# Kernel tuning notes

Measured on AMD Instinct MI355X. Metric: run time of the kernel, lower is better.

## Reference

```python
import jax, jax.numpy as jnp
import numpy as np

# Module hyperparameters
P_, K_, NH = 8, 4, 8
B, H, W, C = 2, 64, 24, 256


def setup_inputs() -> dict:
    key = jax.random.key(0)
    ks = jax.random.split(key, 16)

    def w(k, shape, s=0.02):
        return (jax.random.normal(k, shape) * s).astype(jnp.float32)

    z = lambda *shape: jnp.zeros(shape, jnp.float32)
    return {
        'x_2d': jax.random.normal(ks[0], (B, H, W, C), dtype=jnp.float32),
        # block projections (used as x @ W + b)
        'wq_proj': w(ks[1], (C, C)), 'bq_proj': z(C),
        'wk_proj': w(ks[2], (C, C)), 'bk_proj': z(C),
        'wv_proj': w(ks[3], (C, C)), 'bv_proj': z(C),
        # routing attention projections
        'wq_a': w(ks[4], (C, C)), 'bq_a': z(C),
        'wk_a': w(ks[5], (C, C)), 'bk_a': z(C),
        'wv_a': w(ks[6], (C, C)), 'bv_a': z(C),
        'wo_a': w(ks[7], (C, C)), 'bo_a': z(C),
        # global conv path (HWIO, 5x5, SAME padding == torch padding=2)
        'conv_w': w(ks[8], (5, 5, C, C)), 'conv_b': z(C),
        # layer norms
        'ln1_g': jnp.ones((C,), jnp.float32), 'ln1_b': z(C),
        'ln2_g': jnp.ones((C,), jnp.float32), 'ln2_b': z(C),
    }


def _layer_norm(t, g, b, eps=1e-5):
    m = t.mean(-1, keepdims=True)
    v = ((t - m) ** 2).mean(-1, keepdims=True)
    return (t - m) / jnp.sqrt(v + eps) * g + b


def reference(x_2d, wq_proj, bq_proj, wk_proj, bk_proj, wv_proj, bv_proj,
              wq_a, bq_a, wk_a, bk_a, wv_a, bv_a, wo_a, bo_a,
              conv_w, conv_b, ln1_g, ln1_b, ln2_g, ln2_b):
    Bb, Hh, Ww, Cc = x_2d.shape
    hp = Hh // P_                      # block height
    dk = Cc // NH
    kv = min(K_, P_)

    x_p = x_2d.reshape(Bb, P_, hp, Ww, Cc)
    q_p = x_p @ wq_proj + bq_proj
    k_p = x_p @ wk_proj + bk_proj
    v_p = x_p @ wv_proj + bv_proj

    # block-level routing: mean-pooled block descriptors -> top-k blocks
    q_loc = q_p.mean((2, 3))           # [B,P,C]
    k_loc = k_p.mean((2, 3))
    S_loc = jnp.einsum('bpc,bqc->bpq', q_loc, k_loc)
    _, R = jax.lax.top_k(S_loc, kv)    # [B,P,kv] int32 indices into P

    # gather routed K/V blocks: [B,P,kv,hp*W,C]
    k_flat = k_p.reshape(Bb, P_, hp * Ww, Cc)
    v_flat = v_p.reshape(Bb, P_, hp * Ww, Cc)
    k_fil = jax.vmap(lambda t, r: t[r])(k_flat, R).reshape(Bb, P_, kv, hp, Ww, Cc)
    v_fil = jax.vmap(lambda t, r: t[r])(v_flat, R).reshape(Bb, P_, kv, hp, Ww, Cc)
    q_un = jnp.broadcast_to(q_p[:, :, None], (Bb, P_, kv, hp, Ww, Cc))

    # multi-head attention over flattened (kv*hp*W) per block p
    L = kv * hp * Ww
    def to_heads(t, w, b):
        t = t @ w + b
        t = t.reshape(Bb, P_, kv, hp, Ww, NH, dk)
        return t.transpose(0, 5, 1, 2, 3, 4, 6).reshape(Bb, NH, P_, L, dk)

    qh = to_heads(q_un, wq_a, bq_a)
    kh = to_heads(k_fil, wk_a, bk_a)
    vh = to_heads(v_fil, wv_a, bv_a)

    scores = jnp.einsum('bhpqd,bhpkd->bhpqk', qh, kh) / jnp.sqrt(jnp.float32(dk))
    attn = jax.nn.softmax(scores, axis=-1)
    ctx = jnp.einsum('bhpqk,bhpkd->bhpqd', attn, vh)
    # 'b h p (k hp w) dk -> b p k hp w (h dk)'
    ctx = ctx.reshape(Bb, NH, P_, kv, hp, Ww, dk).transpose(0, 2, 3, 4, 5, 1, 6)
    ctx = ctx.reshape(Bb, P_, kv, hp, Ww, Cc)
    routing_out = (ctx @ wo_a + bo_a).mean(2)          # [B,P,hp,W,C]

    x_res = _layer_norm(x_p + routing_out, ln1_g, ln1_b)

    # global conv path (NHWC SAME conv, kernel 5)
    kv_g = (k_p + v_p).reshape(Bb, Hh, Ww, Cc)
    g = jax.lax.conv_general_dilated(kv_g, conv_w, (1, 1), 'SAME',
                                     dimension_numbers=('NHWC', 'HWIO', 'NHWC')) + conv_b
    g = g.reshape(Bb, P_, hp, Ww, Cc)

    out = _layer_norm(x_res + g, ln2_g, ln2_b)
    return out.reshape(Bb, Hh, Ww, Cc)
```

## Files before the change

### kernel.cpp

```cpp
#include <hip/hip_runtime.h>
#include <hip/hip_bf16.h>


#define NPOS 3072
#define CD   256
#define NE   (NPOS*CD)

typedef short bf16x8 __attribute__((ext_vector_type(8)));
typedef float f32x4  __attribute__((ext_vector_type(4)));

__device__ inline ushort f2bf(float f) {
    __hip_bfloat16 h = __float2bfloat16(f);
    return *reinterpret_cast<ushort*>(&h);
}
__device__ inline float bf2f(ushort u) {
    unsigned v = ((unsigned)u) << 16;
    return *reinterpret_cast<float*>(&v);
}
__device__ inline bf16x8 addbf(bf16x8 a, bf16x8 b) {
    bf16x8 o;
    #pragma unroll
    for (int j = 0; j < 8; ++j)
        o[j] = (short)f2bf(bf2f((ushort)a[j]) + bf2f((ushort)b[j]));
    return o;
}

__global__ __launch_bounds__(256) void wtrans_qkloc(
    const float* __restrict__ w0, const float* __restrict__ w1, const float* __restrict__ w2,
    const float* __restrict__ w3, const float* __restrict__ w4, const float* __restrict__ w5,
    const float* __restrict__ w6, const float* __restrict__ cw,
    ushort* __restrict__ wt, ushort* __restrict__ wct,
    const float* __restrict__ x,
    const float* __restrict__ wq, const float* __restrict__ bq,
    const float* __restrict__ wk, const float* __restrict__ bk,
    float* __restrict__ qloc, float* __restrict__ kloc)
{
    __shared__ float l[64*65];
    int blk = blockIdx.x;
    int tid = threadIdx.x;
    if (blk < 512) {
        const float* M;
        ushort* D;
        int r2;
        if (blk < 112) {
            int mat = blk >> 4; r2 = blk & 15;
            M = mat==0?w0:mat==1?w1:mat==2?w2:mat==3?w3:mat==4?w4:mat==5?w5:w6;
            D = wt + (size_t)mat*65536;
        } else {
            int b2 = blk - 112;
            int tap = b2 >> 4; r2 = b2 & 15;
            M = cw + (size_t)tap*65536;
            D = wct + (size_t)tap*65536;
        }
        int ci0 = (r2 >> 2)*64, co0 = (r2 & 3)*64;
        int a = tid >> 6, c = tid & 63;
        #pragma unroll 4
        for (int k = 0; k < 16; ++k) {
            int cil = k*4 + a;
            l[cil*65 + c] = M[(size_t)(ci0 + cil)*256 + co0 + c];
        }
        __syncthreads();
        #pragma unroll 4
        for (int k = 0; k < 16; ++k) {
            int col = k*4 + a;
            D[((size_t)(co0 + col))*256 + ci0 + c] = f2bf(l[c*65 + col]);
        }
    } else {
        int q2 = blk - 512;
        int bp = q2 & 15, which = q2 >> 4;
        int c = tid;
        float s = 0.f;
        for (int i = 0; i < 192; ++i)
            s += x[((size_t)(bp*192 + i))*256 + c];
        l[c] = s * (1.0f/192.0f);
        __syncthreads();
        const float* W  = which ? wk : wq;
        const float* Bv = which ? bk : bq;
        float* dst      = which ? kloc : qloc;
        float acc = Bv[c];
        #pragma unroll 8
        for (int k = 0; k < 256; ++k)
            acc += l[k] * W[(size_t)k*256 + c];
        dst[bp*256 + c] = acc;
    }
}

__global__ void topk_kern(const float* __restrict__ qloc, const float* __restrict__ kloc,
                          int* __restrict__ Rix)
{
    __shared__ float S[64];
    int b = blockIdx.x, t = threadIdx.x;
    int p = t >> 3, qq = t & 7;
    float s = 0.f;
    for (int c = 0; c < 256; ++c)
        s += qloc[(b*8+p)*256 + c] * kloc[(b*8+qq)*256 + c];
    S[t] = s;
    __syncthreads();
    if (t < 8) {
        float vals[8];
        #pragma unroll
        for (int j = 0; j < 8; ++j) vals[j] = S[t*8 + j];
        for (int j = 0; j < 4; ++j) {
            int best = 0; float bv = vals[0];
            #pragma unroll
            for (int i = 1; i < 8; ++i) if (vals[i] > bv) { bv = vals[i]; best = i; }
            Rix[(b*8 + t)*4 + j] = best;
            vals[best] = -1e30f;
        }
    }
}

__global__ __launch_bounds__(256) void gemm_btx3(
    const float* __restrict__ A,
    const ushort* __restrict__ T0, const ushort* __restrict__ T1, const ushort* __restrict__ T2,
    const float* __restrict__ B0, const float* __restrict__ B1, const float* __restrict__ B2,
    ushort* __restrict__ U0, ushort* __restrict__ U1, ushort* __restrict__ U2)
{
    __shared__ __align__(16) ushort As[32*264];
    int y = blockIdx.y;
    const ushort* T = y==0 ? T0 : (y==1 ? T1 : T2);
    const float* Bi = y==0 ? B0 : (y==1 ? B1 : B2);
    ushort* U = y==0 ? U0 : (y==1 ? U1 : U2);
    int tid = threadIdx.x;
    int m0 = (blockIdx.x >> 1)*32;
    int nh = blockIdx.x & 1;
    #pragma unroll
    for (int i = 0; i < 4; ++i) {
        int c = i*256 + tid;
        int pos = c >> 5, off = (c & 31)*8;
        const float* src = A + (size_t)(m0 + pos)*256 + off;
        float4 v0 = *(const float4*)src;
        float4 v1 = *(const float4*)(src + 4);
        ushort4 o0, o1;
        o0.x = f2bf(v0.x); o0.y = f2bf(v0.y); o0.z = f2bf(v0.z); o0.w = f2bf(v0.w);
        o1.x = f2bf(v1.x); o1.y = f2bf(v1.y); o1.z = f2bf(v1.z); o1.w = f2bf(v1.w);
        *(ushort4*)&As[pos*264 + off]     = o0;
        *(ushort4*)&As[pos*264 + off + 4] = o1;
    }
    __syncthreads();
    int w = tid >> 6, lane = tid & 63, lm = lane & 15, lq = lane >> 4;
    const ushort* tb = T + ((size_t)(nh*128 + w*32 + lm))*256 + lq*8;

    f32x4 acc[2][2];
    #pragma unroll
    for (int mt = 0; mt < 2; ++mt)
        #pragma unroll
        for (int nt = 0; nt < 2; ++nt) acc[mt][nt] = (f32x4){0.f,0.f,0.f,0.f};

    bf16x8 bw[2];
    #pragma unroll
    for (int nt = 0; nt < 2; ++nt) bw[nt] = *(const bf16x8*)(tb + nt*4096);

    for (int kc = 0; kc < 8; ++kc) {
        int nk = (kc + 1 < 8) ? kc + 1 : 7;
        bf16x8 bn[2];
        #pragma unroll
        for (int nt = 0; nt < 2; ++nt) bn[nt] = *(const bf16x8*)(tb + nt*4096 + nk*32);
        bf16x8 af[2];
        #pragma unroll
        for (int mt = 0; mt < 2; ++mt)
            af[mt] = *(const bf16x8*)&As[(mt*16 + lm)*264 + kc*32 + lq*8];
        #pragma unroll
        for (int mt = 0; mt < 2; ++mt)
            #pragma unroll
            for (int nt = 0; nt < 2; ++nt)
                acc[mt][nt] = __builtin_amdgcn_mfma_f32_16x16x32_bf16(af[mt], bw[nt], acc[mt][nt], 0,0,0);
        #pragma unroll
        for (int nt = 0; nt < 2; ++nt) bw[nt] = bn[nt];
    }

    #pragma unroll
    for (int mt = 0; mt < 2; ++mt) {
        #pragma unroll
        for (int nt = 0; nt < 2; ++nt) {
            int n = nh*128 + w*32 + nt*16 + lm;
            float bb = Bi[n];
            #pragma unroll
            for (int j = 0; j < 4; ++j) {
                int m = m0 + mt*16 + lq*4 + j;
                U[(size_t)m*256 + n] = f2bf(acc[mt][nt][j] + bb);
            }
        }
    }
}

__global__ __launch_bounds__(256) void gemm_bt3(
    const ushort* __restrict__ A0, const ushort* __restrict__ A1, const ushort* __restrict__ A2,
    const ushort* __restrict__ T0, const ushort* __restrict__ T1, const ushort* __restrict__ T2,
    const float* __restrict__ B0, const float* __restrict__ B1, const float* __restrict__ B2,
    ushort* __restrict__ U0, ushort* __restrict__ U1, ushort* __restrict__ U2,
    float s0, float s1, float s2)
{
    __shared__ __align__(16) ushort As[32*264];
    int y = blockIdx.y;
    const ushort* A = y==0 ? A0 : (y==1 ? A1 : A2);
    const ushort* T = y==0 ? T0 : (y==1 ? T1 : T2);
    const float* Bi = y==0 ? B0 : (y==1 ? B1 : B2);
    ushort* U = y==0 ? U0 : (y==1 ? U1 : U2);
    float  sc = y==0 ? s0 : (y==1 ? s1 : s2);
    int tid = threadIdx.x;
    int m0 = (blockIdx.x >> 1)*32;
    int nh = blockIdx.x & 1;
    #pragma unroll
    for (int i = 0; i < 4; ++i) {
        int c = i*256 + tid;
        int pos = c >> 5, off = (c & 31)*8;
        *(bf16x8*)&As[pos*264 + off] = *(const bf16x8*)(A + (size_t)(m0 + pos)*256 + off);
    }
    __syncthreads();
    int w = tid >> 6, lane = tid & 63, lm = lane & 15, lq = lane >> 4;
    const ushort* tb = T + ((size_t)(nh*128 + w*32 + lm))*256 + lq*8;

    f32x4 acc[2][2];
    #pragma unroll
    for (int mt = 0; mt < 2; ++mt)
        #pragma unroll
        for (int nt = 0; nt < 2; ++nt) acc[mt][nt] = (f32x4){0.f,0.f,0.f,0.f};

    bf16x8 bw[2];
    #pragma unroll
    for (int nt = 0; nt < 2; ++nt) bw[nt] = *(const bf16x8*)(tb + nt*4096);

    for (int kc = 0; kc < 8; ++kc) {
        int nk = (kc + 1 < 8) ? kc + 1 : 7;
        bf16x8 bn[2];
        #pragma unroll
        for (int nt = 0; nt < 2; ++nt) bn[nt] = *(const bf16x8*)(tb + nt*4096 + nk*32);
        bf16x8 af[2];
        #pragma unroll
        for (int mt = 0; mt < 2; ++mt)
            af[mt] = *(const bf16x8*)&As[(mt*16 + lm)*264 + kc*32 + lq*8];
        #pragma unroll
        for (int mt = 0; mt < 2; ++mt)
            #pragma unroll
            for (int nt = 0; nt < 2; ++nt)
                acc[mt][nt] = __builtin_amdgcn_mfma_f32_16x16x32_bf16(af[mt], bw[nt], acc[mt][nt], 0,0,0);
        #pragma unroll
        for (int nt = 0; nt < 2; ++nt) bw[nt] = bn[nt];
    }

    #pragma unroll
    for (int mt = 0; mt < 2; ++mt) {
        #pragma unroll
        for (int nt = 0; nt < 2; ++nt) {
            int n = nh*128 + w*32 + nt*16 + lm;
            float bb = Bi[n];
            #pragma unroll
            for (int j = 0; j < 4; ++j) {
                int m = m0 + mt*16 + lq*4 + j;
                U[(size_t)m*256 + n] = f2bf((acc[mt][nt][j] + bb) * sc);
            }
        }
    }
}

__global__ __launch_bounds__(256) void attn_conv(
    const ushort* __restrict__ qab, const ushort* __restrict__ kab,
    const ushort* __restrict__ vab, const int* __restrict__ Rix,
    float* __restrict__ pl, ushort* __restrict__ pacc,
    const ushort* __restrict__ kpb, const ushort* __restrict__ vpb,
    const ushort* __restrict__ wct, ushort* __restrict__ pconv)
{
    __shared__ __align__(16) ushort SMEM[19008];
    int tid = threadIdx.x;
    int bid = blockIdx.x;
    if (bid < 640) {
        int ch = bid & 1;
        int t2 = bid >> 1;
        int rp = t2 / 5, dy = t2 - rp*5;
        int b = rp >> 5, y0 = (rp & 31)*2;

        const bf16x8 zero8 = (bf16x8){0,0,0,0,0,0,0,0};
        #pragma unroll
        for (int i = 0; i < 7; ++i) {
            int c = i*256 + tid;
            int row = (c >= 896);
            int cc = c - row*896;
            int pos = cc >> 5, off = (cc & 31)*8;
            int y = y0 + row + dy - 2;
            bf16x8 v = zero8;
            if (y >= 0 && y < 64 && pos >= 2 && pos < 26) {
                size_t sb = ((size_t)((b*64 + y)*24 + (pos - 2)))*256 + off;
                v = addbf(*(const bf16x8*)(kpb + sb), *(const bf16x8*)(vpb + sb));
            }
            *(bf16x8*)(&SMEM[row*9504 + pos*264 + off]) = v;
        }
        __syncthreads();

        int w = tid >> 6;
        int lane = tid & 63, lm = lane & 15, lq = lane >> 4;
        const ushort* bbase = wct + ((size_t)((dy*5)*256 + ch*128 + w*32 + lm))*256 + lq*8;
        const ushort* a00 = &SMEM[lm*264 + lq*8];

        f32x4 acc[2][2][2];
        #pragma unroll
        for (int r = 0; r < 2; ++r)
            #pragma unroll
            for (int mt = 0; mt < 2; ++mt)
                #pragma unroll
                for (int nt = 0; nt < 2; ++nt)
                    acc[r][mt][nt] = (f32x4){0.f,0.f,0.f,0.f};

        bf16x8 b0[2], b1[2];
        #pragma unroll
        for (int nt = 0; nt < 2; ++nt) b0[nt] = *(const bf16x8*)(bbase + nt*4096);
        #pragma unroll
        for (int nt = 0; nt < 2; ++nt) b1[nt] = *(const bf16x8*)(bbase + 32 + nt*4096);

        for (int iter = 0; iter < 40; ++iter) {
            int i2 = (iter + 2 < 40) ? iter + 2 : 39;
            int boff = (i2 >> 3)*65536 + (i2 & 7)*32;
            bf16x8 bn[2];
            #pragma unroll
            for (int nt = 0; nt < 2; ++nt) bn[nt] = *(const bf16x8*)(bbase + boff + nt*4096);

            int aoff = (iter >> 3)*264 + (iter & 7)*32;
            bf16x8 af[2][2];
            #pragma unroll
            for (int r = 0; r < 2; ++r)
                #pragma unroll
                for (int mt = 0; mt < 2; ++mt)
                    af[r][mt] = *(const bf16x8*)(a00 + r*9504 + mt*4224 + aoff);

            #pragma unroll
            for (int r = 0; r < 2; ++r)
                #pragma unroll
                for (int mt = 0; mt < 2; ++mt)
                    #pragma unroll
                    for (int nt = 0; nt < 2; ++nt)
                        acc[r][mt][nt] = __builtin_amdgcn_mfma_f32_16x16x32_bf16(
                            af[r][mt], b0[nt], acc[r][mt][nt], 0, 0, 0);

            #pragma unroll
            for (int nt = 0; nt < 2; ++nt) { b0[nt] = b1[nt]; b1[nt] = bn[nt]; }
        }

        #pragma unroll
        for (int r = 0; r < 2; ++r) {
            int grow = rp*2 + r;
            #pragma unroll
            for (int mt = 0; mt < 2; ++mt) {
                #pragma unroll
                for (int nt = 0; nt < 2; ++nt) {
                    int cob = ch*128 + w*32 + nt*16 + lm;
                    #pragma unroll
                    for (int j = 0; j < 4; ++j) {
                        int x = mt*16 + lq*4 + j;
                        if (x < 24)
                            pconv[((size_t)(dy*3072 + grow*24 + x))*256 + cob]
                                = f2bf(acc[r][mt][nt][j]);
                    }
                }
            }
        }
    } else {
        int id = bid - 640;
        int bph = id >> 2, kvb = id & 3;
        int w = tid >> 6, lane = tid & 63;
        int lm = lane & 15, lq = lane >> 4;
        int bp = bph >> 3, h = bph & 7, b = bp >> 3;
        int r = Rix[bp*4 + kvb];
        int vrow0 = (b*8 + r)*192;
        ushort* P  = SMEM;
        ushort* Vs = SMEM + 2560;

        #pragma unroll
        for (int i = 0; i < 6; ++i) {
            int idx = i*256 + tid;
            int pos = idx >> 3, c4 = (idx & 7)*4;
            ushort4 v = *(const ushort4*)(vab + ((size_t)(vrow0 + pos))*256 + h*32 + c4);
            Vs[(c4+0)*200 + pos] = v.x;
            Vs[(c4+1)*200 + pos] = v.y;
            Vs[(c4+2)*200 + pos] = v.z;
            Vs[(c4+3)*200 + pos] = v.w;
        }

        bf16x8 qf[3];
        #pragma unroll
        for (int t = 0; t < 3; ++t)
            qf[t] = *(const bf16x8*)(qab + ((size_t)(bp*192 + w*48 + t*16 + lm))*256 + h*32 + lq*8);

        const ushort* kbase = kab + ((size_t)(vrow0))*256 + h*32 + lq*8;
        ushort* pw = P + w*640;
        __syncthreads();

        f32x4 O[3][2];
        #pragma unroll
        for (int t = 0; t < 3; ++t) { O[t][0] = (f32x4){0,0,0,0}; O[t][1] = (f32x4){0,0,0,0}; }
        float l[3] = {0.f, 0.f, 0.f};

        for (int k0 = 0; k0 < 192; k0 += 32) {
            bf16x8 kf0 = *(const bf16x8*)(kbase + (size_t)(k0 + lm)*256);
            bf16x8 kf1 = *(const bf16x8*)(kbase + (size_t)(k0 + 16 + lm)*256);
            bf16x8 vf0 = *(const bf16x8*)(&Vs[lm*200 + k0 + lq*8]);
            bf16x8 vf1 = *(const bf16x8*)(&Vs[(16 + lm)*200 + k0 + lq*8]);
            #pragma unroll
            for (int t = 0; t < 3; ++t) {
                f32x4 s0 = __builtin_amdgcn_mfma_f32_16x16x32_bf16(kf0, qf[t], (f32x4){0,0,0,0}, 0,0,0);
                f32x4 s1 = __builtin_amdgcn_mfma_f32_16x16x32_bf16(kf1, qf[t], (f32x4){0,0,0,0}, 0,0,0);
                float p0[4], p1[4];
                #pragma unroll
                for (int j = 0; j < 4; ++j) { p0[j] = __expf(s0[j]); p1[j] = __expf(s1[j]); }
                l[t] += p0[0]+p0[1]+p0[2]+p0[3] + p1[0]+p1[1]+p1[2]+p1[3];
                ushort4 a, c;
                a.x = f2bf(p0[0]); a.y = f2bf(p0[1]); a.z = f2bf(p0[2]); a.w = f2bf(p0[3]);
                c.x = f2bf(p1[0]); c.y = f2bf(p1[1]); c.z = f2bf(p1[2]); c.w = f2bf(p1[3]);
                *(ushort4*)(pw + lm*40 + lq*4)      = a;
                *(ushort4*)(pw + lm*40 + 16 + lq*4) = c;
                bf16x8 pf = *(const bf16x8*)(pw + lm*40 + lq*8);
                O[t][0] = __builtin_amdgcn_mfma_f32_16x16x32_bf16(pf, vf0, O[t][0], 0,0,0);
                O[t][1] = __builtin_amdgcn_mfma_f32_16x16x32_bf16(pf, vf1, O[t][1], 0,0,0);
            }
        }

        #pragma unroll
        for (int t = 0; t < 3; ++t) {
            float lt = l[t];
            lt += __shfl_xor(lt, 16);
            lt += __shfl_xor(lt, 32);
            size_t pbase = ((size_t)(bph*4 + kvb))*192 + w*48 + t*16;
            if (lq == 0) pl[pbase + lm] = lt;
            #pragma unroll
            for (int nt = 0; nt < 2; ++nt)
                #pragma unroll
                for (int reg = 0; reg < 4; ++reg)
                    pacc[(pbase + lq*4 + reg)*32 + nt*16 + lm] = f2bf(O[t][nt][reg]);
        }
    }
}

__global__ __launch_bounds__(256) void gemm_wo_ln2(
    const float* __restrict__ pl, const ushort* __restrict__ pacc,
    const ushort* __restrict__ T, const float* __restrict__ boa,
    const float* __restrict__ x,
    const float* __restrict__ g1, const float* __restrict__ b1,
    const ushort* __restrict__ pc, const float* __restrict__ cb,
    const float* __restrict__ g2, const float* __restrict__ b2,
    float* __restrict__ out)
{
    __shared__ __align__(16) ushort As[32*264];
    __shared__ float L2x[32*256];
    int tid = threadIdx.x;
    int m0 = blockIdx.x*32;
    #pragma unroll
    for (int i = 0; i < 4; ++i) {
        int c = i*256 + tid;
        int pos = c >> 5, off = (c & 31)*8;
        int m = m0 + pos;
        int bp = m / 192, q = m - bp*192;
        int h = off >> 5, d0 = off & 31;
        int bph = bp*8 + h;
        float ls = 0.f;
        float cv[8] = {0,0,0,0,0,0,0,0};
        #pragma unroll
        for (int k = 0; k < 4; ++k) {
            size_t pidx = ((size_t)(bph*4 + k))*192 + q;
            ls += pl[pidx];
            bf16x8 pv = *(const bf16x8*)(pacc + pidx*32 + d0);
            #pragma unroll
            for (int j = 0; j < 8; ++j) cv[j] += bf2f((ushort)pv[j]);
        }
        ushort o[8];
        #pragma unroll
        for (int j = 0; j < 8; ++j) o[j] = f2bf(cv[j] / ls);
        *(ushort4*)&As[pos*264 + off]     = make_ushort4(o[0],o[1],o[2],o[3]);
        *(ushort4*)&As[pos*264 + off + 4] = make_ushort4(o[4],o[5],o[6],o[7]);
    }
    __syncthreads();
    int w = tid >> 6, lane = tid & 63, lm = lane & 15, lq = lane >> 4;
    const ushort* tb = T + ((size_t)(w*64 + lm))*256 + lq*8;

    f32x4 acc[2][4];
    #pragma unroll
    for (int mt = 0; mt < 2; ++mt)
        #pragma unroll
        for (int nt = 0; nt < 4; ++nt) acc[mt][nt] = (f32x4){0.f,0.f,0.f,0.f};

    bf16x8 bw[4];
    #pragma unroll
    for (int nt = 0; nt < 4; ++nt) bw[nt] = *(const bf16x8*)(tb + nt*4096);

    for (int kc = 0; kc < 8; ++kc) {
        int nk = (kc + 1 < 8) ? kc + 1 : 7;
        bf16x8 bn[4];
        #pragma unroll
        for (int nt = 0; nt < 4; ++nt) bn[nt] = *(const bf16x8*)(tb + nt*4096 + nk*32);
        bf16x8 af[2];
        #pragma unroll
        for (int mt = 0; mt < 2; ++mt)
            af[mt] = *(const bf16x8*)&As[(mt*16 + lm)*264 + kc*32 + lq*8];
        #pragma unroll
        for (int mt = 0; mt < 2; ++mt)
            #pragma unroll
            for (int nt = 0; nt < 4; ++nt)
                acc[mt][nt] = __builtin_amdgcn_mfma_f32_16x16x32_bf16(af[mt], bw[nt], acc[mt][nt], 0,0,0);
        #pragma unroll
        for (int nt = 0; nt < 4; ++nt) bw[nt] = bn[nt];
    }

    #pragma unroll
    for (int mt = 0; mt < 2; ++mt) {
        #pragma unroll
        for (int nt = 0; nt < 4; ++nt) {
            int n = w*64 + nt*16 + lm;
            float bb = boa[n];
            #pragma unroll
            for (int j = 0; j < 4; ++j) {
                int pos = mt*16 + lq*4 + j;
                float val = acc[mt][nt][j] + bb;
                L2x[pos*256 + n] = val + x[(size_t)(m0 + pos)*256 + n];
            }
        }
    }
    __syncthreads();
    #pragma unroll
    for (int rr = 0; rr < 8; ++rr) {
        int pos = w*8 + rr;
        int grow = m0 + pos;
        float4 a = *(const float4*)(&L2x[pos*256 + lane*4]);
        float x0 = a.x, x1 = a.y, x2 = a.z, x3 = a.w;
        float s  = x0 + x1 + x2 + x3;
        float sq = x0*x0 + x1*x1 + x2*x2 + x3*x3;
        #pragma unroll
        for (int off = 32; off > 0; off >>= 1) {
            s  += __shfl_xor(s,  off);
            sq += __shfl_xor(sq, off);
        }
        float mean = s * (1.0f/256.0f);
        float var  = sq * (1.0f/256.0f) - mean*mean;
        float rstd = rsqrtf(var + 1e-5f);
        float4 gv = *(const float4*)(g1 + lane*4);
        float4 bv = *(const float4*)(b1 + lane*4);
        float r0 = (x0 - mean)*rstd*gv.x + bv.x;
        float r1 = (x1 - mean)*rstd*gv.y + bv.y;
        float r2 = (x2 - mean)*rstd*gv.z + bv.z;
        float r3 = (x3 - mean)*rstd*gv.w + bv.w;
        size_t base = (size_t)grow*256 + lane*4;
        float4 gsum = *(const float4*)(cb + lane*4);
        #pragma unroll
        for (int d = 0; d < 5; ++d) {
            ushort4 v = *(const ushort4*)(pc + (size_t)d*NE + base);
            gsum.x += bf2f(v.x); gsum.y += bf2f(v.y);
            gsum.z += bf2f(v.z); gsum.w += bf2f(v.w);
        }
        float y0 = r0 + gsum.x, y1 = r1 + gsum.y, y2 = r2 + gsum.z, y3 = r3 + gsum.w;
        float s2v  = y0 + y1 + y2 + y3;
        float sq2  = y0*y0 + y1*y1 + y2*y2 + y3*y3;
        #pragma unroll
        for (int off = 32; off > 0; off >>= 1) {
            s2v += __shfl_xor(s2v, off);
            sq2 += __shfl_xor(sq2, off);
        }
        float mean2 = s2v * (1.0f/256.0f);
        float var2  = sq2 * (1.0f/256.0f) - mean2*mean2;
        float rstd2 = rsqrtf(var2 + 1e-5f);
        float4 g2v = *(const float4*)(g2 + lane*4);
        float4 b2v = *(const float4*)(b2 + lane*4);
        float4 o;
        o.x = (y0 - mean2)*rstd2*g2v.x + b2v.x;
        o.y = (y1 - mean2)*rstd2*g2v.y + b2v.y;
        o.z = (y2 - mean2)*rstd2*g2v.z + b2v.z;
        o.w = (y3 - mean2)*rstd2*g2v.w + b2v.w;
        *(float4*)(out + base) = o;
    }
}

extern "C" void kernel_launch(void* const* d_in, const int* in_sizes, int n_in,
                              void* d_out, int out_size, void* d_ws, size_t ws_size,
                              hipStream_t stream)
{
    (void)in_sizes; (void)n_in; (void)out_size; (void)ws_size;
    const float* x    = (const float*)d_in[0];
    const float* wq   = (const float*)d_in[1];
    const float* bq   = (const float*)d_in[2];
    const float* wk   = (const float*)d_in[3];
    const float* bk   = (const float*)d_in[4];
    const float* wv   = (const float*)d_in[5];
    const float* bv   = (const float*)d_in[6];
    const float* wqa  = (const float*)d_in[7];
    const float* bqa  = (const float*)d_in[8];
    const float* wka  = (const float*)d_in[9];
    const float* bka  = (const float*)d_in[10];
    const float* wva  = (const float*)d_in[11];
    const float* bva  = (const float*)d_in[12];
    const float* woa  = (const float*)d_in[13];
    const float* boa  = (const float*)d_in[14];
    const float* cw   = (const float*)d_in[15];
    const float* cbi  = (const float*)d_in[16];
    const float* ln1g = (const float*)d_in[17];
    const float* ln1b = (const float*)d_in[18];
    const float* ln2g = (const float*)d_in[19];
    const float* ln2b = (const float*)d_in[20];
    float* out = (float*)d_out;

    float* ws = (float*)d_ws;
    const size_t HNE = NE/2;
    ushort* qpb = (ushort*)(ws + 0*HNE);
    ushort* kpb = (ushort*)(ws + 1*HNE);
    ushort* vpb = (ushort*)(ws + 3*HNE);
    ushort* qab = (ushort*)(ws + 4*HNE);
    ushort* kab = (ushort*)(ws + 5*HNE);
    ushort* vab = (ushort*)(ws + 6*HNE);
    float* R    = ws + 8*HNE;
    ushort* pacc = (ushort*)R;
    float*  pl   = R + 1572864;
    ushort* pconv= (ushort*)(R + 1671168);
    ushort* wt7 = (ushort*)(R + 3932160);
    ushort* wct = (ushort*)(R + 3932160 + 229376);
    float* qloc = R + 3932160 + 229376 + 819200;
    float* kloc = qloc + 4096;
    int*   Rix  = (int*)(kloc + 4096);

    wtrans_qkloc<<<544, 256, 0, stream>>>(wq,wk,wv,wqa,wka,wva,woa, cw, wt7, wct,
                                          x, wq,bq, wk,bk, qloc, kloc);
    topk_kern<<<2, 64, 0, stream>>>(qloc, kloc, Rix);
    gemm_btx3<<<dim3(192,3), 256, 0, stream>>>(
        x, wt7, wt7+65536, wt7+131072, bq,bk,bv, qpb,kpb,vpb);
    gemm_bt3<<<dim3(192,3), 256, 0, stream>>>(
        qpb,kpb,vpb, wt7+196608, wt7+262144, wt7+327680, bqa,bka,bva,
        qab,kab,vab, 0.17677669529663687f,1.f,1.f);
    attn_conv<<<1152, 256, 0, stream>>>(qab, kab, vab, Rix, pl, pacc,
                                        kpb, vpb, wct, pconv);
    gemm_wo_ln2<<<96, 256, 0, stream>>>(pl, pacc, wt7+393216, boa, x, ln1g, ln1b,
                                        pconv, cbi, ln2g, ln2b, out);
}
```

Before: 203.9 us.

## Compose chained projection weights to remove the second GEMM pass

The two back-to-back linear projections (x@Wq then @Wq_a, likewise for k and v) are folded into single composed weight matrices, computed once per call by a small weight-GEMM kernel, along with composed biases. A fourth output computes k+v directly with the summed weight (Wk+Wv) for the conv path. This replaces two activation GEMM passes with one and drops the intermediate q/k/v buffers and the elementwise k+v add in the conv loader. In exchange it adds a weight-composition kernel, and the composed weights rounded to bf16 change rounding behaviour.

```diff
diff --git a/kernel.cpp b/kernel.cpp
--- a/kernel.cpp
+++ b/kernel.cpp
@@ -25,14 +25,13 @@
     return o;
 }
 
-__global__ __launch_bounds__(256) void wtrans_qkloc(
+__global__ __launch_bounds__(256) void wtransA(
     const float* __restrict__ w0, const float* __restrict__ w1, const float* __restrict__ w2,
     const float* __restrict__ w3, const float* __restrict__ w4, const float* __restrict__ w5,
     const float* __restrict__ w6, const float* __restrict__ cw,
-    ushort* __restrict__ wt, ushort* __restrict__ wct,
+    ushort* __restrict__ wt, ushort* __restrict__ wct, ushort* __restrict__ wstr,
     const float* __restrict__ x,
-    const float* __restrict__ wq, const float* __restrict__ bq,
-    const float* __restrict__ wk, const float* __restrict__ bk,
+    const float* __restrict__ bq, const float* __restrict__ bk,
     float* __restrict__ qloc, float* __restrict__ kloc)
 {
     __shared__ float l[64*65];
@@ -65,8 +64,21 @@
             int col = k*4 + a;
             D[((size_t)(co0 + col))*256 + ci0 + c] = f2bf(l[c*65 + col]);
         }
+    } else if (blk < 524) {
+        int b2 = blk - 512;
+        int mat = b2 >> 2, quarter = b2 & 3;
+        const float* M = mat==0 ? w0 : (mat==1 ? w1 : w2);
+        size_t base = (size_t)quarter*16384;
+        #pragma unroll
+        for (int i = 0; i < 16; ++i) {
+            size_t idx = base + (size_t)i*1024 + tid*4;
+            float4 v = *(const float4*)(M + idx);
+            ushort4 o;
+            o.x = f2bf(v.x); o.y = f2bf(v.y); o.z = f2bf(v.z); o.w = f2bf(v.w);
+            *(ushort4*)(wstr + (size_t)mat*65536 + idx) = o;
+        }
     } else {
-        int q2 = blk - 512;
+        int q2 = blk - 524;
         int bp = q2 & 15, which = q2 >> 4;
         int c = tid;
         float s = 0.f;
@@ -74,7 +86,7 @@
             s += x[((size_t)(bp*192 + i))*256 + c];
         l[c] = s * (1.0f/192.0f);
         __syncthreads();
-        const float* W  = which ? wk : wq;
+        const float* W  = which ? w1 : w0;
         const float* Bv = which ? bk : bq;
         float* dst      = which ? kloc : qloc;
         float acc = Bv[c];
@@ -82,6 +94,85 @@
         for (int k = 0; k < 256; ++k)
             acc += l[k] * W[(size_t)k*256 + c];
         dst[bp*256 + c] = acc;
+    }
+}
+
+__global__ __launch_bounds__(256) void compose(
+    const ushort* __restrict__ wt7, const ushort* __restrict__ wstr,
+    const float* __restrict__ bq, const float* __restrict__ bk, const float* __restrict__ bv,
+    const float* __restrict__ bqa, const float* __restrict__ bka, const float* __restrict__ bva,
+    ushort* __restrict__ wtc, ushort* __restrict__ wtkv, float* __restrict__ bcomp)
+{
+    int y = blockIdx.y;
+    int tid = threadIdx.x;
+    if (y < 3) {
+        __shared__ __align__(16) ushort As[32*264];
+        const ushort* A = wt7 + (size_t)(3 + y)*65536;
+        const ushort* T = wstr + (size_t)y*65536;
+        ushort* U = wtc + (size_t)y*65536;
+        int m0 = (blockIdx.x >> 1)*32;
+        int nh = blockIdx.x & 1;
+        #pragma unroll
+        for (int i = 0; i < 4; ++i) {
+            int c = i*256 + tid;
+            int pos = c >> 5, off = (c & 31)*8;
+            *(bf16x8*)&As[pos*264 + off] = *(const bf16x8*)(A + (size_t)(m0 + pos)*256 + off);
+        }
+        __syncthreads();
+        int w = tid >> 6, lane = tid & 63, lm = lane & 15, lq = lane >> 4;
+        const ushort* tb = T + ((size_t)(nh*128 + w*32 + lm))*256 + lq*8;
+        f32x4 acc[2][2];
+        #pragma unroll
+        for (int mt = 0; mt < 2; ++mt)
+            #pragma unroll
+            for (int nt = 0; nt < 2; ++nt) acc[mt][nt] = (f32x4){0.f,0.f,0.f,0.f};
+        for (int kc = 0; kc < 8; ++kc) {
+            bf16x8 bw[2];
+            #pragma unroll
+            for (int nt = 0; nt < 2; ++nt) bw[nt] = *(const bf16x8*)(tb + nt*4096 + kc*32);
+            bf16x8 af[2];
+            #pragma unroll
+            for (int mt = 0; mt < 2; ++mt)
+                af[mt] = *(const bf16x8*)&As[(mt*16 + lm)*264 + kc*32 + lq*8];
+            #pragma unroll
+            for (int mt = 0; mt < 2; ++mt)
+                #pragma unroll
+                for (int nt = 0; nt < 2; ++nt)
+                    acc[mt][nt] = __builtin_amdgcn_mfma_f32_16x16x32_bf16(af[mt], bw[nt], acc[mt][nt], 0,0,0);
+        }
+        #pragma unroll
+        for (int mt = 0; mt < 2; ++mt)
+            #pragma unroll
+            for (int nt = 0; nt < 2; ++nt) {
+                int n = nh*128 + w*32 + nt*16 + lm;
+                #pragma unroll
+                for (int j = 0; j < 4; ++j) {
+                    int m = m0 + mt*16 + lq*4 + j;
+                    U[(size_t)m*256 + n] = f2bf(acc[mt][nt][j]);
+                }
+            }
+    } else {
+        const ushort* wk7 = wt7 + 65536;
+        const ushort* wv7 = wt7 + 131072;
+        size_t base = (size_t)blockIdx.x*4096 + tid*16;
+        #pragma unroll
+        for (int i = 0; i < 2; ++i) {
+            bf16x8 a = *(const bf16x8*)(wk7 + base + i*8);
+            bf16x8 b = *(const bf16x8*)(wv7 + base + i*8);
+            *(bf16x8*)(wtkv + base + i*8) = addbf(a, b);
+        }
+        int bx = blockIdx.x;
+        if (bx < 3) {
+            const float* bsrc = bx==0 ? bq : (bx==1 ? bk : bv);
+            const float* basr = bx==0 ? bqa : (bx==1 ? bka : bva);
+            const ushort* wa = wt7 + (size_t)(3 + bx)*65536;
+            float s = basr[tid];
+            for (int k = 0; k < 256; ++k)
+                s += bsrc[k] * bf2f(wa[(size_t)tid*256 + k]);
+            bcomp[bx*256 + tid] = s;
+        } else if (bx == 3) {
+            bcomp[3*256 + tid] = bk[tid] + bv[tid];
+        }
     }
 }
 
@@ -110,17 +201,19 @@
     }
 }
 
-__global__ __launch_bounds__(256) void gemm_btx3(
+__global__ __launch_bounds__(256) void gemm_quad(
     const float* __restrict__ A,
-    const ushort* __restrict__ T0, const ushort* __restrict__ T1, const ushort* __restrict__ T2,
-    const float* __restrict__ B0, const float* __restrict__ B1, const float* __restrict__ B2,
-    ushort* __restrict__ U0, ushort* __restrict__ U1, ushort* __restrict__ U2)
+    const ushort* __restrict__ wtc, const ushort* __restrict__ wtkv,
+    const float* __restrict__ bcomp,
+    ushort* __restrict__ U0, ushort* __restrict__ U1,
+    ushort* __restrict__ U2, ushort* __restrict__ U3)
 {
     __shared__ __align__(16) ushort As[32*264];
     int y = blockIdx.y;
-    const ushort* T = y==0 ? T0 : (y==1 ? T1 : T2);
-    const float* Bi = y==0 ? B0 : (y==1 ? B1 : B2);
-    ushort* U = y==0 ? U0 : (y==1 ? U1 : U2);
+    const ushort* T = (y < 3) ? (wtc + (size_t)y*65536) : wtkv;
+    const float* Bi = bcomp + y*256;
+    ushort* U = y==0 ? U0 : (y==1 ? U1 : (y==2 ? U2 : U3));
+    float sc = (y == 0) ? 0.17677669529663687f : 1.0f;
     int tid = threadIdx.x;
     int m0 = (blockIdx.x >> 1)*32;
     int nh = blockIdx.x & 1;
@@ -178,76 +271,6 @@
             #pragma unroll
             for (int j = 0; j < 4; ++j) {
                 int m = m0 + mt*16 + lq*4 + j;
-                U[(size_t)m*256 + n] = f2bf(acc[mt][nt][j] + bb);
-            }
-        }
-    }
-}
-
-__global__ __launch_bounds__(256) void gemm_bt3(
-    const ushort* __restrict__ A0, const ushort* __restrict__ A1, const ushort* __restrict__ A2,
-    const ushort* __restrict__ T0, const ushort* __restrict__ T1, const ushort* __restrict__ T2,
-    const float* __restrict__ B0, const float* __restrict__ B1, const float* __restrict__ B2,
-    ushort* __restrict__ U0, ushort* __restrict__ U1, ushort* __restrict__ U2,
-    float s0, float s1, float s2)
-{
-    __shared__ __align__(16) ushort As[32*264];
-    int y = blockIdx.y;
-    const ushort* A = y==0 ? A0 : (y==1 ? A1 : A2);
-    const ushort* T = y==0 ? T0 : (y==1 ? T1 : T2);
-    const float* Bi = y==0 ? B0 : (y==1 ? B1 : B2);
-    ushort* U = y==0 ? U0 : (y==1 ? U1 : U2);
-    float  sc = y==0 ? s0 : (y==1 ? s1 : s2);
-    int tid = threadIdx.x;
-    int m0 = (blockIdx.x >> 1)*32;
-    int nh = blockIdx.x & 1;
-    #pragma unroll
-    for (int i = 0; i < 4; ++i) {
-        int c = i*256 + tid;
-        int pos = c >> 5, off = (c & 31)*8;
-        *(bf16x8*)&As[pos*264 + off] = *(const bf16x8*)(A + (size_t)(m0 + pos)*256 + off);
-    }
-    __syncthreads();
-    int w = tid >> 6, lane = tid & 63, lm = lane & 15, lq = lane >> 4;
-    const ushort* tb = T + ((size_t)(nh*128 + w*32 + lm))*256 + lq*8;
-
-    f32x4 acc[2][2];
-    #pragma unroll
-    for (int mt = 0; mt < 2; ++mt)
-        #pragma unroll
-        for (int nt = 0; nt < 2; ++nt) acc[mt][nt] = (f32x4){0.f,0.f,0.f,0.f};
-
-    bf16x8 bw[2];
-    #pragma unroll
-    for (int nt = 0; nt < 2; ++nt) bw[nt] = *(const bf16x8*)(tb + nt*4096);
-
-    for (int kc = 0; kc < 8; ++kc) {
-        int nk = (kc + 1 < 8) ? kc + 1 : 7;
-        bf16x8 bn[2];
-        #pragma unroll
-        for (int nt = 0; nt < 2; ++nt) bn[nt] = *(const bf16x8*)(tb + nt*4096 + nk*32);
-        bf16x8 af[2];
-        #pragma unroll
-        for (int mt = 0; mt < 2; ++mt)
-            af[mt] = *(const bf16x8*)&As[(mt*16 + lm)*264 + kc*32 + lq*8];
-        #pragma unroll
-        for (int mt = 0; mt < 2; ++mt)
-            #pragma unroll
-            for (int nt = 0; nt < 2; ++nt)
-                acc[mt][nt] = __builtin_amdgcn_mfma_f32_16x16x32_bf16(af[mt], bw[nt], acc[mt][nt], 0,0,0);
-        #pragma unroll
-        for (int nt = 0; nt < 2; ++nt) bw[nt] = bn[nt];
-    }
-
-    #pragma unroll
-    for (int mt = 0; mt < 2; ++mt) {
-        #pragma unroll
-        for (int nt = 0; nt < 2; ++nt) {
-            int n = nh*128 + w*32 + nt*16 + lm;
-            float bb = Bi[n];
-            #pragma unroll
-            for (int j = 0; j < 4; ++j) {
-                int m = m0 + mt*16 + lq*4 + j;
                 U[(size_t)m*256 + n] = f2bf((acc[mt][nt][j] + bb) * sc);
             }
         }
@@ -258,7 +281,7 @@
     const ushort* __restrict__ qab, const ushort* __restrict__ kab,
     const ushort* __restrict__ vab, const int* __restrict__ Rix,
     float* __restrict__ pl, ushort* __restrict__ pacc,
-    const ushort* __restrict__ kpb, const ushort* __restrict__ vpb,
+    const ushort* __restrict__ kvc,
     const ushort* __restrict__ wct, ushort* __restrict__ pconv)
 {
     __shared__ __align__(16) ushort SMEM[19008];
@@ -281,7 +304,7 @@
             bf16x8 v = zero8;
             if (y >= 0 && y < 64 && pos >= 2 && pos < 26) {
                 size_t sb = ((size_t)((b*64 + y)*24 + (pos - 2)))*256 + off;
-                v = addbf(*(const bf16x8*)(kpb + sb), *(const bf16x8*)(vpb + sb));
+                v = *(const bf16x8*)(kvc + sb);
             }
             *(bf16x8*)(&SMEM[row*9504 + pos*264 + off]) = v;
         }
@@ -595,32 +618,31 @@
 
     float* ws = (float*)d_ws;
     const size_t HNE = NE/2;
-    ushort* qpb = (ushort*)(ws + 0*HNE);
-    ushort* kpb = (ushort*)(ws + 1*HNE);
-    ushort* vpb = (ushort*)(ws + 3*HNE);
-    ushort* qab = (ushort*)(ws + 4*HNE);
-    ushort* kab = (ushort*)(ws + 5*HNE);
-    ushort* vab = (ushort*)(ws + 6*HNE);
-    float* R    = ws + 8*HNE;
+    ushort* qab = (ushort*)(ws + 0*HNE);
+    ushort* kab = (ushort*)(ws + 1*HNE);
+    ushort* vab = (ushort*)(ws + 2*HNE);
+    ushort* kvc = (ushort*)(ws + 3*HNE);
+    float* R    = ws + 4*HNE;
     ushort* pacc = (ushort*)R;
     float*  pl   = R + 1572864;
     ushort* pconv= (ushort*)(R + 1671168);
-    ushort* wt7 = (ushort*)(R + 3932160);
-    ushort* wct = (ushort*)(R + 3932160 + 229376);
-    float* qloc = R + 3932160 + 229376 + 819200;
-    float* kloc = qloc + 4096;
-    int*   Rix  = (int*)(kloc + 4096);
-
-    wtrans_qkloc<<<544, 256, 0, stream>>>(wq,wk,wv,wqa,wka,wva,woa, cw, wt7, wct,
-                                          x, wq,bq, wk,bk, qloc, kloc);
+    ushort* wt7  = (ushort*)(R + 3637248);
+    ushort* wstr = wt7 + 458752;
+    ushort* wtc  = wstr + 196608;
+    ushort* wtkv = wtc + 196608;
+    ushort* wct  = wtkv + 65536;
+    float* bcomp = (float*)(wct + 1638400);
+    float* qloc  = bcomp + 1024;
+    float* kloc  = qloc + 4096;
+    int*   Rix   = (int*)(kloc + 4096);
+
+    wtransA<<<556, 256, 0, stream>>>(wq,wk,wv,wqa,wka,wva,woa, cw, wt7, wct, wstr,
+                                     x, bq, bk, qloc, kloc);
+    compose<<<dim3(16,4), 256, 0, stream>>>(wt7, wstr, bq,bk,bv, bqa,bka,bva,
+                                            wtc, wtkv, bcomp);
     topk_kern<<<2, 64, 0, stream>>>(qloc, kloc, Rix);
-    gemm_btx3<<<dim3(192,3), 256, 0, stream>>>(
-        x, wt7, wt7+65536, wt7+131072, bq,bk,bv, qpb,kpb,vpb);
-    gemm_bt3<<<dim3(192,3), 256, 0, stream>>>(
-        qpb,kpb,vpb, wt7+196608, wt7+262144, wt7+327680, bqa,bka,bva,
-        qab,kab,vab, 0.17677669529663687f,1.f,1.f);
-    attn_conv<<<1152, 256, 0, stream>>>(qab, kab, vab, Rix, pl, pacc,
-                                        kpb, vpb, wct, pconv);
-    gemm_wo_ln2<<<96, 256, 0, stream>>>(pl, pacc, wt7+393216, boa, x, ln1g, ln1b,
+    gemm_quad<<<dim3(192,4), 256, 0, stream>>>(x, wtc, wtkv, bcomp, qab, kab, vab, kvc);
+    attn_conv<<<1152, 256, 0, stream>>>(qab, kab, vab, Rix, pl, pacc, kvc, wct, pconv);
+    gemm_wo_ln2<<<96, 256, 0, stream>>>(pl, pacc, wt7 + 393216, boa, x, ln1g, ln1b,
                                         pconv, cbi, ln2g, ln2b, out);
 }
```

New measurement: 199.9 us. 2.0% less time.
